# Kernel tuning notes

Measured on AMD Instinct MI355X. Metric: run time of the kernel, lower is better.

The kernel has to match this reference:

```python
import jax, jax.numpy as jnp
import numpy as np

N = 50000
E = 800000
NEG_SLOPE = 0.2


def setup_inputs() -> dict:
    key = jax.random.key(0)
    ks = jax.random.split(key, 12)
    feat = jax.random.normal(ks[0], (N, 256), dtype=jnp.float32)
    src = jax.random.randint(ks[1], (E,), 0, N, dtype=jnp.int32)
    dst = jax.random.randint(ks[2], (E,), 0, N, dtype=jnp.int32)
    # layer 1: in=256 -> H=4, D=64 (concat 256)
    W1 = jax.random.normal(ks[3], (256, 256), dtype=jnp.float32) * (1.0 / np.sqrt(256))
    attn_l1 = jax.random.normal(ks[4], (4, 64), dtype=jnp.float32) * 0.1
    attn_r1 = jax.random.normal(ks[5], (4, 64), dtype=jnp.float32) * 0.1
    bias1 = jnp.zeros((256,), dtype=jnp.float32)
    # layer 2: in=256 -> H=1, D=128
    W2 = jax.random.normal(ks[6], (256, 128), dtype=jnp.float32) * (1.0 / np.sqrt(256))
    attn_l2 = jax.random.normal(ks[7], (1, 128), dtype=jnp.float32) * 0.1
    attn_r2 = jax.random.normal(ks[8], (1, 128), dtype=jnp.float32) * 0.1
    bias2 = jnp.zeros((128,), dtype=jnp.float32)
    return {"feat": feat, "src": src, "dst": dst,
            "W1": W1, "attn_l1": attn_l1, "attn_r1": attn_r1, "bias1": bias1,
            "W2": W2, "attn_l2": attn_l2, "attn_r2": attn_r2, "bias2": bias2}


def gat_conv(feat, src, dst, W, attn_l, attn_r, bias, apply_relu):
    H, D = attn_l.shape
    n = feat.shape[0]
    ft = (feat @ W).reshape(n, H, D)                      # [N,H,D]
    el = jnp.einsum('nhd,hd->nh', ft, attn_l)             # [N,H]
    er = jnp.einsum('nhd,hd->nh', ft, attn_r)             # [N,H]
    e = el[src] + er[dst]                                 # [E,H]  u_add_v
    e = jnp.where(e > 0, e, NEG_SLOPE * e)                # leaky_relu
    # edge softmax grouped by dst
    m = jax.ops.segment_max(e, dst, num_segments=n)       # [N,H]
    ex = jnp.exp(e - m[dst])
    denom = jax.ops.segment_sum(ex, dst, num_segments=n)  # [N,H]
    a = ex / denom[dst]                                   # [E,H]
    msg = ft[src] * a[:, :, None]                         # [E,H,D]
    out = jax.ops.segment_sum(msg, dst, num_segments=n)   # [N,H,D]
    out = out + bias.reshape(1, H, D)
    out = out.reshape(n, H * D)                           # concat_out
    if apply_relu:
        out = jax.nn.relu(out)
    return out


def reference(feat, src, dst, W1, attn_l1, attn_r1, bias1, W2, attn_l2, attn_r2, bias2):
    h = gat_conv(feat, src, dst, W1, attn_l1, attn_r1, bias1, apply_relu=True)
    h = gat_conv(h, src, dst, W2, attn_l2, attn_r2, bias2, apply_relu=False)
    return h
```

## Files before the change

kernel.cpp:

```cpp
#include <hip/hip_runtime.h>
#include <hip/hip_bf16.h>

#define NEG_SLOPE 0.2f

typedef short s16x8 __attribute__((ext_vector_type(8)));
typedef float f32x4 __attribute__((ext_vector_type(4)));

__device__ __forceinline__ unsigned short f2bf(float f) {
    unsigned int u = __float_as_uint(f);
    unsigned int r = (u + 0x7fffu + ((u >> 16) & 1u)) >> 16;
    return (unsigned short)r;
}
__device__ __forceinline__ float bf2f(unsigned int us) {
    return __uint_as_float(us << 16);
}


__global__ void count_k(const int* __restrict__ dst, int* __restrict__ counts, int E) {
    int e = blockIdx.x * blockDim.x + threadIdx.x;
    if (e < E) atomicAdd(&counts[dst[e]], 1);
}

__global__ __launch_bounds__(1024) void partial_k(const int* __restrict__ counts,
                                                  int* __restrict__ part, int n) {
    __shared__ int s[16];
    int tid = threadIdx.x, lane = tid & 63, wid = tid >> 6;
    int i = blockIdx.x * 1024 + tid;
    int v = (i < n) ? counts[i] : 0;
    #pragma unroll
    for (int o = 32; o > 0; o >>= 1) v += __shfl_xor(v, o);
    if (lane == 0) s[wid] = v;
    __syncthreads();
    if (tid == 0) {
        int r = 0;
        #pragma unroll
        for (int w = 0; w < 16; w++) r += s[w];
        part[blockIdx.x] = r;
    }
}

__global__ void scanpart_k(int* __restrict__ part, int nb) {
    int tid = threadIdx.x;
    int orig = (tid < nb) ? part[tid] : 0;
    int v = orig;
    #pragma unroll
    for (int o = 1; o < 64; o <<= 1) {
        int t = __shfl_up(v, o);
        if (tid >= o) v += t;
    }
    if (tid < nb) part[tid] = v - orig;
}

__global__ __launch_bounds__(1024) void scanwrite_k(const int* __restrict__ counts,
                                                    const int* __restrict__ part,
                                                    int* __restrict__ offsets,
                                                    int* __restrict__ cursor, int n) {
    __shared__ int s_wt[16];
    int tid = threadIdx.x, lane = tid & 63, wid = tid >> 6;
    int i = blockIdx.x * 1024 + tid;
    int v = (i < n) ? counts[i] : 0;
    int incl = v;
    #pragma unroll
    for (int o = 1; o < 64; o <<= 1) {
        int t = __shfl_up(incl, o);
        if (lane >= o) incl += t;
    }
    if (lane == 63) s_wt[wid] = incl;
    __syncthreads();
    if (tid == 0) {
        int r = 0;
        #pragma unroll
        for (int w = 0; w < 16; w++) { int t = s_wt[w]; s_wt[w] = r; r += t; }
    }
    __syncthreads();
    if (i < n) {
        int excl = part[blockIdx.x] + s_wt[wid] + incl - v;
        offsets[i + 1] = excl + v;
        cursor[i] = excl;
    }
    if (blockIdx.x == 0 && tid == 0) offsets[0] = 0;
}

__global__ void fill_csr_k(const int* __restrict__ src, const int* __restrict__ dst,
                           int* __restrict__ cursor, int* __restrict__ csr_src, int E) {
    int e = blockIdx.x * blockDim.x + threadIdx.x;
    if (e < E) {
        int pos = atomicAdd(&cursor[dst[e]], 1);
        csr_src[pos] = src[e];
    }
}


__global__ __launch_bounds__(256) void gemm_k(const float* __restrict__ A,
                                              const float* __restrict__ B,
                                              unsigned short* __restrict__ Cb,
                                              int M, int K, int Nc) {
    __shared__ __align__(16) unsigned short As_hi[128][40], As_lo[128][40];
    __shared__ __align__(16) unsigned short Bs_hi[64][40],  Bs_lo[64][40];

    const int tid = threadIdx.x;
    const int lane = tid & 63, wid = tid >> 6;
    const int row0 = blockIdx.x * 128;
    const int col0 = blockIdx.y * 64;
    const int wm = (wid & 1) * 64;
    const int wn = (wid >> 1) * 32;
    const int quad = lane >> 4, mrow = lane & 15;

    const int a_r = tid >> 1;
    const int a_k = (tid & 1) * 16;
    const int b_k = tid >> 3;
    const int b_n = (tid & 7) * 8;
    const bool a_valid = (row0 + a_r) < M;

    f32x4 acc[4][2];
    #pragma unroll
    for (int i = 0; i < 4; i++)
        #pragma unroll
        for (int j = 0; j < 2; j++) acc[i][j] = f32x4{0.f, 0.f, 0.f, 0.f};

    for (int k0 = 0; k0 < K; k0 += 32) {
        float af[16];
        if (a_valid) {
            const float* ap = &A[(size_t)(row0 + a_r) * K + k0 + a_k];
            #pragma unroll
            for (int q = 0; q < 4; q++) {
                float4 t = *(const float4*)(ap + q * 4);
                af[q * 4 + 0] = t.x; af[q * 4 + 1] = t.y;
                af[q * 4 + 2] = t.z; af[q * 4 + 3] = t.w;
            }
        } else {
            #pragma unroll
            for (int q = 0; q < 16; q++) af[q] = 0.f;
        }
        unsigned int* dh = (unsigned int*)&As_hi[a_r][a_k];
        unsigned int* dl = (unsigned int*)&As_lo[a_r][a_k];
        #pragma unroll
        for (int p = 0; p < 8; p++) {
            unsigned short h0 = f2bf(af[2 * p]), h1 = f2bf(af[2 * p + 1]);
            unsigned short l0 = f2bf(af[2 * p] - bf2f(h0));
            unsigned short l1 = f2bf(af[2 * p + 1] - bf2f(h1));
            dh[p] = (unsigned int)h0 | ((unsigned int)h1 << 16);
            dl[p] = (unsigned int)l0 | ((unsigned int)l1 << 16);
        }
        {
            const float* bp = &B[(size_t)(k0 + b_k) * Nc + col0 + b_n];
            float4 t0 = *(const float4*)(bp);
            float4 t1 = *(const float4*)(bp + 4);
            float bf[8] = {t0.x, t0.y, t0.z, t0.w, t1.x, t1.y, t1.z, t1.w};
            #pragma unroll
            for (int x = 0; x < 8; x++) {
                unsigned short h = f2bf(bf[x]);
                unsigned short l = f2bf(bf[x] - bf2f(h));
                Bs_hi[b_n + x][b_k] = h;
                Bs_lo[b_n + x][b_k] = l;
            }
        }
        __syncthreads();

        s16x8 ah[4], al[4], bh[2], bl[2];
        #pragma unroll
        for (int i = 0; i < 4; i++) {
            ah[i] = *(const s16x8*)&As_hi[wm + 16 * i + mrow][quad * 8];
            al[i] = *(const s16x8*)&As_lo[wm + 16 * i + mrow][quad * 8];
        }
        #pragma unroll
        for (int j = 0; j < 2; j++) {
            bh[j] = *(const s16x8*)&Bs_hi[wn + 16 * j + mrow][quad * 8];
            bl[j] = *(const s16x8*)&Bs_lo[wn + 16 * j + mrow][quad * 8];
        }
        #pragma unroll
        for (int i = 0; i < 4; i++)
            #pragma unroll
            for (int j = 0; j < 2; j++) {
                acc[i][j] = __builtin_amdgcn_mfma_f32_16x16x32_bf16(ah[i], bh[j], acc[i][j], 0, 0, 0);
                acc[i][j] = __builtin_amdgcn_mfma_f32_16x16x32_bf16(ah[i], bl[j], acc[i][j], 0, 0, 0);
                acc[i][j] = __builtin_amdgcn_mfma_f32_16x16x32_bf16(al[i], bh[j], acc[i][j], 0, 0, 0);
            }
        __syncthreads();
    }

    #pragma unroll
    for (int i = 0; i < 4; i++) {
        #pragma unroll
        for (int j = 0; j < 2; j++) {
            int col = col0 + wn + 16 * j + mrow;
            int rbase = row0 + wm + 16 * i + quad * 4;
            #pragma unroll
            for (int r = 0; r < 4; r++) {
                int row = rbase + r;
                if (row < M) Cb[(size_t)row * Nc + col] = f2bf(acc[i][j][r]);
            }
        }
    }
}


template <int H, int D>
__global__ __launch_bounds__(256) void eler_k(const unsigned short* __restrict__ ft,
                                              const float* __restrict__ attn_l,
                                              const float* __restrict__ attn_r,
                                              float* __restrict__ el,
                                              float* __restrict__ er, int n_nodes) {
    constexpr int HD = H * D;
    constexpr int CPL = HD / 64;
    constexpr int G = 64 / H;
    __shared__ float s_al[HD], s_ar[HD];
    const int tid = threadIdx.x;
    for (int i = tid; i < HD; i += 256) { s_al[i] = attn_l[i]; s_ar[i] = attn_r[i]; }
    __syncthreads();
    const int lane = tid & 63, wid = tid >> 6;
    const int n = blockIdx.x * 4 + wid;
    if (n >= n_nodes) return;
    const int c0 = lane * CPL;
    const int head = c0 / D;
    float f[CPL];
    if constexpr (CPL == 4) {
        uint2 u = ((const uint2*)ft)[(size_t)n * (HD / 4) + lane];
        f[0] = bf2f(u.x & 0xffff); f[1] = bf2f(u.x >> 16);
        f[2] = bf2f(u.y & 0xffff); f[3] = bf2f(u.y >> 16);
    } else {
        unsigned int u = ((const unsigned int*)ft)[(size_t)n * (HD / 2) + lane];
        f[0] = bf2f(u & 0xffff); f[1] = bf2f(u >> 16);
    }
    float vl = 0.f, vr = 0.f;
    #pragma unroll
    for (int t = 0; t < CPL; t++) {
        vl = fmaf(f[t], s_al[c0 + t], vl);
        vr = fmaf(f[t], s_ar[c0 + t], vr);
    }
    #pragma unroll
    for (int o = G / 2; o > 0; o >>= 1) {
        vl += __shfl_xor(vl, o);
        vr += __shfl_xor(vr, o);
    }
    if ((lane & (G - 1)) == 0) {
        el[n * H + head] = vl;
        er[n * H + head] = vr;
    }
}


template <int H>
__device__ __forceinline__ void edge_e(const float* __restrict__ el, int sv,
                                       const float* ern, float* e) {
    if constexpr (H == 4) {
        float4 e4 = ((const float4*)el)[sv];
        float tmp[4] = {e4.x, e4.y, e4.z, e4.w};
        #pragma unroll
        for (int h = 0; h < 4; h++) {
            float t = tmp[h] + ern[h];
            e[h] = t > 0.f ? t : NEG_SLOPE * t;
        }
    } else {
        float t = el[sv] + ern[0];
        e[0] = t > 0.f ? t : NEG_SLOPE * t;
    }
}

template <int H, int CPL>
__device__ __forceinline__ void gather_edges(const unsigned short* __restrict__ ft,
                                             const int* s_src_w, const float* s_a_w,
                                             int cnt, int lane, int h_of, float* acc) {
    int i = 0;
    if constexpr (CPL == 4) {
        const uint2* fp = ((const uint2*)ft) + lane;
        for (; i + 8 <= cnt; i += 8) {
            int ss[8]; float ww[8]; uint2 uu[8];
            #pragma unroll
            for (int u = 0; u < 8; u++) { ss[u] = s_src_w[i + u]; ww[u] = s_a_w[(i + u) * H + h_of]; }
            #pragma unroll
            for (int u = 0; u < 8; u++) uu[u] = fp[(size_t)ss[u] * 64];
            #pragma unroll
            for (int u = 0; u < 8; u++) {
                acc[0] = fmaf(ww[u], bf2f(uu[u].x & 0xffff), acc[0]);
                acc[1] = fmaf(ww[u], bf2f(uu[u].x >> 16), acc[1]);
                acc[2] = fmaf(ww[u], bf2f(uu[u].y & 0xffff), acc[2]);
                acc[3] = fmaf(ww[u], bf2f(uu[u].y >> 16), acc[3]);
            }
        }
        for (; i < cnt; i++) {
            float w = s_a_w[i * H + h_of];
            uint2 u = fp[(size_t)s_src_w[i] * 64];
            acc[0] = fmaf(w, bf2f(u.x & 0xffff), acc[0]);
            acc[1] = fmaf(w, bf2f(u.x >> 16), acc[1]);
            acc[2] = fmaf(w, bf2f(u.y & 0xffff), acc[2]);
            acc[3] = fmaf(w, bf2f(u.y >> 16), acc[3]);
        }
    } else {
        const unsigned int* fp = ((const unsigned int*)ft) + lane;
        for (; i + 8 <= cnt; i += 8) {
            int ss[8]; float ww[8]; unsigned int uu[8];
            #pragma unroll
            for (int u = 0; u < 8; u++) { ss[u] = s_src_w[i + u]; ww[u] = s_a_w[(i + u) * H + h_of]; }
            #pragma unroll
            for (int u = 0; u < 8; u++) uu[u] = fp[(size_t)ss[u] * 64];
            #pragma unroll
            for (int u = 0; u < 8; u++) {
                acc[0] = fmaf(ww[u], bf2f(uu[u] & 0xffff), acc[0]);
                acc[1] = fmaf(ww[u], bf2f(uu[u] >> 16), acc[1]);
            }
        }
        for (; i < cnt; i++) {
            float w = s_a_w[i * H + h_of];
            unsigned int u = fp[(size_t)s_src_w[i] * 64];
            acc[0] = fmaf(w, bf2f(u & 0xffff), acc[0]);
            acc[1] = fmaf(w, bf2f(u >> 16), acc[1]);
        }
    }
}

template <int H, int D, bool RELU>
__global__ __launch_bounds__(256) void fagg_k(const unsigned short* __restrict__ ft,
                                              const float* __restrict__ el,
                                              const float* __restrict__ er,
                                              const int* __restrict__ offsets,
                                              const int* __restrict__ csr_src,
                                              const float* __restrict__ bias,
                                              float* __restrict__ out, int n_nodes) {
    constexpr int HD = H * D;
    constexpr int CPL = HD / 64;
    const int lane = threadIdx.x & 63;
    const int w = threadIdx.x >> 6;
    const int n = blockIdx.x * 4 + w;
    __shared__ int   s_src[4][64];
    __shared__ float s_a[4][64 * H];
    if (n >= n_nodes) return;
    const int off = offsets[n];
    const int deg = offsets[n + 1] - off;
    const int c0 = lane * CPL;
    const int h_of = c0 / D;

    float ern[H];
    #pragma unroll
    for (int h = 0; h < H; h++) ern[h] = er[n * H + h];

    float acc[CPL];
    #pragma unroll
    for (int t = 0; t < CPL; t++) acc[t] = 0.f;

    const int* s_src_w = s_src[w];
    const float* s_a_w = s_a[w];

    if (deg > 0 && deg <= 64) {
        const bool act = lane < deg;
        int sv = 0;
        float ev[H];
        #pragma unroll
        for (int h = 0; h < H; h++) ev[h] = -1e30f;
        if (act) {
            sv = csr_src[off + lane];
            edge_e<H>(el, sv, ern, ev);
        }
        float m[H];
        #pragma unroll
        for (int h = 0; h < H; h++) m[h] = ev[h];
        #pragma unroll
        for (int h = 0; h < H; h++)
            for (int o = 32; o > 0; o >>= 1) m[h] = fmaxf(m[h], __shfl_xor(m[h], o));
        float ex[H], sm[H];
        #pragma unroll
        for (int h = 0; h < H; h++) { ex[h] = act ? __expf(ev[h] - m[h]) : 0.f; sm[h] = ex[h]; }
        #pragma unroll
        for (int h = 0; h < H; h++)
            for (int o = 32; o > 0; o >>= 1) sm[h] += __shfl_xor(sm[h], o);
        if (act) {
            s_src[w][lane] = sv;
            #pragma unroll
            for (int h = 0; h < H; h++)
                s_a[w][lane * H + h] = ex[h] * (sm[h] > 0.f ? 1.f / sm[h] : 0.f);
        }
        gather_edges<H, CPL>(ft, s_src_w, s_a_w, deg, lane, h_of, acc);
    } else if (deg > 64) {
        float m[H];
        #pragma unroll
        for (int h = 0; h < H; h++) m[h] = -1e30f;
        for (int i = lane; i < deg; i += 64) {
            float e[H];
            edge_e<H>(el, csr_src[off + i], ern, e);
            #pragma unroll
            for (int h = 0; h < H; h++) m[h] = fmaxf(m[h], e[h]);
        }
        #pragma unroll
        for (int h = 0; h < H; h++)
            for (int o = 32; o > 0; o >>= 1) m[h] = fmaxf(m[h], __shfl_xor(m[h], o));
        float sm[H];
        #pragma unroll
        for (int h = 0; h < H; h++) sm[h] = 0.f;
        for (int i = lane; i < deg; i += 64) {
            float e[H];
            edge_e<H>(el, csr_src[off + i], ern, e);
            #pragma unroll
            for (int h = 0; h < H; h++) sm[h] += __expf(e[h] - m[h]);
        }
        #pragma unroll
        for (int h = 0; h < H; h++)
            for (int o = 32; o > 0; o >>= 1) sm[h] += __shfl_xor(sm[h], o);
        float inv[H];
        #pragma unroll
        for (int h = 0; h < H; h++) inv[h] = (sm[h] > 0.f) ? (1.f / sm[h]) : 0.f;
        for (int base = 0; base < deg; base += 64) {
            int cnt = min(64, deg - base);
            if (lane < cnt) {
                int sv = csr_src[off + base + lane];
                float e[H];
                edge_e<H>(el, sv, ern, e);
                s_src[w][lane] = sv;
                #pragma unroll
                for (int h = 0; h < H; h++)
                    s_a[w][lane * H + h] = __expf(e[h] - m[h]) * inv[h];
            }
            gather_edges<H, CPL>(ft, s_src_w, s_a_w, cnt, lane, h_of, acc);
        }
    }

    if constexpr (CPL == 4) {
        float4 b4 = ((const float4*)bias)[lane];
        float v0 = acc[0] + b4.x, v1 = acc[1] + b4.y, v2 = acc[2] + b4.z, v3 = acc[3] + b4.w;
        if (RELU) { v0 = fmaxf(v0, 0.f); v1 = fmaxf(v1, 0.f); v2 = fmaxf(v2, 0.f); v3 = fmaxf(v3, 0.f); }
        ((float4*)out)[(size_t)n * 64 + lane] = float4{v0, v1, v2, v3};
    } else {
        float2 b2 = ((const float2*)bias)[lane];
        float v0 = acc[0] + b2.x, v1 = acc[1] + b2.y;
        if (RELU) { v0 = fmaxf(v0, 0.f); v1 = fmaxf(v1, 0.f); }
        ((float2*)out)[(size_t)n * 64 + lane] = float2{v0, v1};
    }
}


extern "C" void kernel_launch(void* const* d_in, const int* in_sizes, int n_in,
                              void* d_out, int out_size, void* d_ws, size_t ws_size,
                              hipStream_t stream) {
    const float* feat    = (const float*)d_in[0];
    const int*   src     = (const int*)d_in[1];
    const int*   dst     = (const int*)d_in[2];
    const float* W1      = (const float*)d_in[3];
    const float* attn_l1 = (const float*)d_in[4];
    const float* attn_r1 = (const float*)d_in[5];
    const float* bias1   = (const float*)d_in[6];
    const float* W2      = (const float*)d_in[7];
    const float* attn_l2 = (const float*)d_in[8];
    const float* attn_r2 = (const float*)d_in[9];
    const float* bias2   = (const float*)d_in[10];
    float* out = (float*)d_out;

    const int N = in_sizes[0] / 256;
    const int E = in_sizes[1];
    const int NB = (N + 1023) / 1024;

    char* ws = (char*)d_ws;
    size_t o = 0;
    auto alloc = [&](size_t bytes) -> void* {
        void* p = ws + o;
        o = (o + bytes + 255) & ~(size_t)255;
        return p;
    };
    int* counts  = (int*)alloc((size_t)N * 4);
    int* cursor  = (int*)alloc((size_t)N * 4);
    int* offsets = (int*)alloc((size_t)(N + 1) * 4);
    int* part    = (int*)alloc(64 * 4);
    int* csr_src = (int*)alloc((size_t)E * 4);
    float* el1 = (float*)alloc((size_t)N * 4 * 4);
    float* er1 = (float*)alloc((size_t)N * 4 * 4);
    float* el2 = (float*)alloc((size_t)N * 4);
    float* er2 = (float*)alloc((size_t)N * 4);
    unsigned short* ft1b = (unsigned short*)alloc((size_t)N * 256 * 2);
    float* h1 = (float*)alloc((size_t)N * 256 * 4);
    unsigned short* ft2b = ft1b;

    hipMemsetAsync(counts, 0, (size_t)N * 4, stream);
    count_k<<<(E + 255) / 256, 256, 0, stream>>>(dst, counts, E);
    partial_k<<<NB, 1024, 0, stream>>>(counts, part, N);
    scanpart_k<<<1, 64, 0, stream>>>(part, NB);
    scanwrite_k<<<NB, 1024, 0, stream>>>(counts, part, offsets, cursor, N);
    fill_csr_k<<<(E + 255) / 256, 256, 0, stream>>>(src, dst, cursor, csr_src, E);

    gemm_k<<<dim3((N + 127) / 128, 256 / 64), 256, 0, stream>>>(feat, W1, ft1b, N, 256, 256);
    eler_k<4, 64><<<(N + 3) / 4, 256, 0, stream>>>(ft1b, attn_l1, attn_r1, el1, er1, N);
    fagg_k<4, 64, true><<<(N + 3) / 4, 256, 0, stream>>>(ft1b, el1, er1, offsets, csr_src, bias1, h1, N);

    gemm_k<<<dim3((N + 127) / 128, 128 / 64), 256, 0, stream>>>(h1, W2, ft2b, N, 256, 128);
    eler_k<1, 128><<<(N + 3) / 4, 256, 0, stream>>>(ft2b, attn_l2, attn_r2, el2, er2, N);
    fagg_k<1, 128, false><<<(N + 3) / 4, 256, 0, stream>>>(ft2b, el2, er2, offsets, csr_src, bias2, out, N);
}
```

Measured before the change: 402.6 us.

## Fold attention projections into GEMM, single-pass scan, prefetch gathers in aggregation

Precomputes W·attn_l and W·attn_r vectors inside the counting kernel, then has each GEMM block compute el/er directly from the fp32 input rows. This removes the separate eler kernels and changes numerics slightly, since el/er now come from fp32 rather than the bf16 outputs. The three-kernel scan is replaced by a single decoupled-lookback scan that spins on per-block flags, which relies on all scan blocks being co-resident. The aggregation kernel now prefetches the first eight neighbour feature rows before the softmax reductions to hide gather latency.

After: 401.2 us. About the same (-0.4%).

```diff
diff --git a/kernel.cpp b/kernel.cpp
--- a/kernel.cpp
+++ b/kernel.cpp
@@ -16,48 +16,51 @@
 }
 
 
-__global__ void count_k(const int* __restrict__ dst, int* __restrict__ counts, int E) {
-    int e = blockIdx.x * blockDim.x + threadIdx.x;
+__global__ void count_wl_k(const int* __restrict__ dst, int* __restrict__ counts, int E,
+                           const float* __restrict__ W1, const float* __restrict__ al1,
+                           const float* __restrict__ ar1,
+                           const float* __restrict__ W2, const float* __restrict__ al2,
+                           const float* __restrict__ ar2,
+                           float* __restrict__ wl1, float* __restrict__ wl2) {
+    if (blockIdx.x == 0) {
+        int k = threadIdx.x;
+        #pragma unroll
+        for (int h = 0; h < 4; h++) {
+            float sl = 0.f, sr = 0.f;
+            #pragma unroll 8
+            for (int d = 0; d < 64; d++) {
+                float wv = W1[k * 256 + h * 64 + d];
+                sl = fmaf(wv, al1[h * 64 + d], sl);
+                sr = fmaf(wv, ar1[h * 64 + d], sr);
+            }
+            wl1[k * 8 + h] = sl;
+            wl1[k * 8 + 4 + h] = sr;
+        }
+        float sl = 0.f, sr = 0.f;
+        #pragma unroll 8
+        for (int d = 0; d < 128; d++) {
+            float wv = W2[k * 128 + d];
+            sl = fmaf(wv, al2[d], sl);
+            sr = fmaf(wv, ar2[d], sr);
+        }
+        wl2[k * 2 + 0] = sl;
+        wl2[k * 2 + 1] = sr;
+        return;
+    }
+    int e = (blockIdx.x - 1) * 256 + threadIdx.x;
     if (e < E) atomicAdd(&counts[dst[e]], 1);
 }
 
-__global__ __launch_bounds__(1024) void partial_k(const int* __restrict__ counts,
-                                                  int* __restrict__ part, int n) {
-    __shared__ int s[16];
-    int tid = threadIdx.x, lane = tid & 63, wid = tid >> 6;
-    int i = blockIdx.x * 1024 + tid;
-    int v = (i < n) ? counts[i] : 0;
-    #pragma unroll
-    for (int o = 32; o > 0; o >>= 1) v += __shfl_xor(v, o);
-    if (lane == 0) s[wid] = v;
-    __syncthreads();
-    if (tid == 0) {
-        int r = 0;
-        #pragma unroll
-        for (int w = 0; w < 16; w++) r += s[w];
-        part[blockIdx.x] = r;
-    }
-}
-
-__global__ void scanpart_k(int* __restrict__ part, int nb) {
-    int tid = threadIdx.x;
-    int orig = (tid < nb) ? part[tid] : 0;
-    int v = orig;
-    #pragma unroll
-    for (int o = 1; o < 64; o <<= 1) {
-        int t = __shfl_up(v, o);
-        if (tid >= o) v += t;
-    }
-    if (tid < nb) part[tid] = v - orig;
-}
-
-__global__ __launch_bounds__(1024) void scanwrite_k(const int* __restrict__ counts,
-                                                    const int* __restrict__ part,
-                                                    int* __restrict__ offsets,
-                                                    int* __restrict__ cursor, int n) {
+
+__global__ __launch_bounds__(1024) void scan_k(const int* __restrict__ counts,
+                                               int* __restrict__ flags,
+                                               int* __restrict__ offsets,
+                                               int* __restrict__ cursor, int n) {
     __shared__ int s_wt[16];
-    int tid = threadIdx.x, lane = tid & 63, wid = tid >> 6;
-    int i = blockIdx.x * 1024 + tid;
+    __shared__ int s_base;
+    const int tid = threadIdx.x, lane = tid & 63, wid = tid >> 6;
+    const int bid = blockIdx.x;
+    const int i = bid * 1024 + tid;
     int v = (i < n) ? counts[i] : 0;
     int incl = v;
     #pragma unroll
@@ -71,14 +74,28 @@
         int r = 0;
         #pragma unroll
         for (int w = 0; w < 16; w++) { int t = s_wt[w]; s_wt[w] = r; r += t; }
+        atomicExch(&flags[bid], r + 1);
+        s_base = 0;
+    }
+    __syncthreads();
+    if (wid == 0) {
+        int contrib = 0;
+        if (lane < bid) {
+            int f;
+            while ((f = atomicAdd(&flags[lane], 0)) == 0) {}
+            contrib = f - 1;
+        }
+        #pragma unroll
+        for (int o = 32; o > 0; o >>= 1) contrib += __shfl_xor(contrib, o);
+        if (lane == 0) s_base = contrib;
     }
     __syncthreads();
     if (i < n) {
-        int excl = part[blockIdx.x] + s_wt[wid] + incl - v;
+        int excl = s_base + s_wt[wid] + (incl - v);
         offsets[i + 1] = excl + v;
         cursor[i] = excl;
     }
-    if (blockIdx.x == 0 && tid == 0) offsets[0] = 0;
+    if (bid == 0 && tid == 0) offsets[0] = 0;
 }
 
 __global__ void fill_csr_k(const int* __restrict__ src, const int* __restrict__ dst,
@@ -91,17 +108,24 @@
 }
 
 
+template <int MODE>
 __global__ __launch_bounds__(256) void gemm_k(const float* __restrict__ A,
                                               const float* __restrict__ B,
                                               unsigned short* __restrict__ Cb,
-                                              int M, int K, int Nc) {
+                                              int M, int K, int Nc,
+                                              const float* __restrict__ wl,
+                                              float* __restrict__ el,
+                                              float* __restrict__ er) {
     __shared__ __align__(16) unsigned short As_hi[128][40], As_lo[128][40];
     __shared__ __align__(16) unsigned short Bs_hi[64][40],  Bs_lo[64][40];
+    __shared__ float s_wla[256], s_wlb[256];
+    __shared__ float s_red[128][2];
 
     const int tid = threadIdx.x;
     const int lane = tid & 63, wid = tid >> 6;
     const int row0 = blockIdx.x * 128;
-    const int col0 = blockIdx.y * 64;
+    const int by = blockIdx.y;
+    const int col0 = by * 64;
     const int wm = (wid & 1) * 64;
     const int wn = (wid >> 1) * 32;
     const int quad = lane >> 4, mrow = lane & 15;
@@ -112,11 +136,16 @@
     const int b_n = (tid & 7) * 8;
     const bool a_valid = (row0 + a_r) < M;
 
+    if (MODE == 1) { s_wla[tid] = wl[tid * 8 + by]; s_wlb[tid] = wl[tid * 8 + 4 + by]; }
+    else           { s_wla[tid] = wl[tid * 2 + by]; }
+    __syncthreads();
+
     f32x4 acc[4][2];
     #pragma unroll
     for (int i = 0; i < 4; i++)
         #pragma unroll
         for (int j = 0; j < 2; j++) acc[i][j] = f32x4{0.f, 0.f, 0.f, 0.f};
+    float pa = 0.f, pb = 0.f;
 
     for (int k0 = 0; k0 < K; k0 += 32) {
         float af[16];
@@ -131,6 +160,11 @@
         } else {
             #pragma unroll
             for (int q = 0; q < 16; q++) af[q] = 0.f;
+        }
+        #pragma unroll
+        for (int p = 0; p < 16; p++) {
+            pa = fmaf(af[p], s_wla[k0 + a_k + p], pa);
+            if (MODE == 1) pb = fmaf(af[p], s_wlb[k0 + a_k + p], pb);
         }
         unsigned int* dh = (unsigned int*)&As_hi[a_r][a_k];
         unsigned int* dl = (unsigned int*)&As_lo[a_r][a_k];
@@ -157,11 +191,11 @@
         }
         __syncthreads();
 
-        s16x8 ah[4], al[4], bh[2], bl[2];
+        s16x8 ah[4], al4[4], bh[2], bl[2];
         #pragma unroll
         for (int i = 0; i < 4; i++) {
-            ah[i] = *(const s16x8*)&As_hi[wm + 16 * i + mrow][quad * 8];
-            al[i] = *(const s16x8*)&As_lo[wm + 16 * i + mrow][quad * 8];
+            ah[i]  = *(const s16x8*)&As_hi[wm + 16 * i + mrow][quad * 8];
+            al4[i] = *(const s16x8*)&As_lo[wm + 16 * i + mrow][quad * 8];
         }
         #pragma unroll
         for (int j = 0; j < 2; j++) {
@@ -172,11 +206,24 @@
         for (int i = 0; i < 4; i++)
             #pragma unroll
             for (int j = 0; j < 2; j++) {
-                acc[i][j] = __builtin_amdgcn_mfma_f32_16x16x32_bf16(ah[i], bh[j], acc[i][j], 0, 0, 0);
-                acc[i][j] = __builtin_amdgcn_mfma_f32_16x16x32_bf16(ah[i], bl[j], acc[i][j], 0, 0, 0);
-                acc[i][j] = __builtin_amdgcn_mfma_f32_16x16x32_bf16(al[i], bh[j], acc[i][j], 0, 0, 0);
+                acc[i][j] = __builtin_amdgcn_mfma_f32_16x16x32_bf16(ah[i],  bh[j], acc[i][j], 0, 0, 0);
+                acc[i][j] = __builtin_amdgcn_mfma_f32_16x16x32_bf16(ah[i],  bl[j], acc[i][j], 0, 0, 0);
+                acc[i][j] = __builtin_amdgcn_mfma_f32_16x16x32_bf16(al4[i], bh[j], acc[i][j], 0, 0, 0);
             }
         __syncthreads();
+    }
+
+    if (a_k == 16) { s_red[a_r][0] = pa; if (MODE == 1) s_red[a_r][1] = pb; }
+    __syncthreads();
+    if (a_k == 0 && a_valid) {
+        float ra = pa + s_red[a_r][0];
+        if (MODE == 1) {
+            float rb = pb + s_red[a_r][1];
+            el[(row0 + a_r) * 4 + by] = ra;
+            er[(row0 + a_r) * 4 + by] = rb;
+        } else {
+            (by == 0 ? el : er)[row0 + a_r] = ra;
+        }
     }
 
     #pragma unroll
@@ -191,51 +238,6 @@
                 if (row < M) Cb[(size_t)row * Nc + col] = f2bf(acc[i][j][r]);
             }
         }
-    }
-}
-
-
-template <int H, int D>
-__global__ __launch_bounds__(256) void eler_k(const unsigned short* __restrict__ ft,
-                                              const float* __restrict__ attn_l,
-                                              const float* __restrict__ attn_r,
-                                              float* __restrict__ el,
-                                              float* __restrict__ er, int n_nodes) {
-    constexpr int HD = H * D;
-    constexpr int CPL = HD / 64;
-    constexpr int G = 64 / H;
-    __shared__ float s_al[HD], s_ar[HD];
-    const int tid = threadIdx.x;
-    for (int i = tid; i < HD; i += 256) { s_al[i] = attn_l[i]; s_ar[i] = attn_r[i]; }
-    __syncthreads();
-    const int lane = tid & 63, wid = tid >> 6;
-    const int n = blockIdx.x * 4 + wid;
-    if (n >= n_nodes) return;
-    const int c0 = lane * CPL;
-    const int head = c0 / D;
-    float f[CPL];
-    if constexpr (CPL == 4) {
-        uint2 u = ((const uint2*)ft)[(size_t)n * (HD / 4) + lane];
-        f[0] = bf2f(u.x & 0xffff); f[1] = bf2f(u.x >> 16);
-        f[2] = bf2f(u.y & 0xffff); f[3] = bf2f(u.y >> 16);
-    } else {
-        unsigned int u = ((const unsigned int*)ft)[(size_t)n * (HD / 2) + lane];
-        f[0] = bf2f(u & 0xffff); f[1] = bf2f(u >> 16);
-    }
-    float vl = 0.f, vr = 0.f;
-    #pragma unroll
-    for (int t = 0; t < CPL; t++) {
-        vl = fmaf(f[t], s_al[c0 + t], vl);
-        vr = fmaf(f[t], s_ar[c0 + t], vr);
-    }
-    #pragma unroll
-    for (int o = G / 2; o > 0; o >>= 1) {
-        vl += __shfl_xor(vl, o);
-        vr += __shfl_xor(vr, o);
-    }
-    if ((lane & (G - 1)) == 0) {
-        el[n * H + head] = vl;
-        er[n * H + head] = vr;
     }
 }
 
@@ -260,16 +262,19 @@
 template <int H, int CPL>
 __device__ __forceinline__ void gather_edges(const unsigned short* __restrict__ ft,
                                              const int* s_src_w, const float* s_a_w,
-                                             int cnt, int lane, int h_of, float* acc) {
-    int i = 0;
+                                             int i0, int cnt, int lane, int h_of,
+                                             float* acc) {
+    int i = i0;
     if constexpr (CPL == 4) {
         const uint2* fp = ((const uint2*)ft) + lane;
         for (; i + 8 <= cnt; i += 8) {
             int ss[8]; float ww[8]; uint2 uu[8];
             #pragma unroll
-            for (int u = 0; u < 8; u++) { ss[u] = s_src_w[i + u]; ww[u] = s_a_w[(i + u) * H + h_of]; }
+            for (int u = 0; u < 8; u++) ss[u] = s_src_w[i + u];
             #pragma unroll
             for (int u = 0; u < 8; u++) uu[u] = fp[(size_t)ss[u] * 64];
+            #pragma unroll
+            for (int u = 0; u < 8; u++) ww[u] = s_a_w[(i + u) * H + h_of];
             #pragma unroll
             for (int u = 0; u < 8; u++) {
                 acc[0] = fmaf(ww[u], bf2f(uu[u].x & 0xffff), acc[0]);
@@ -291,9 +296,11 @@
         for (; i + 8 <= cnt; i += 8) {
             int ss[8]; float ww[8]; unsigned int uu[8];
             #pragma unroll
-            for (int u = 0; u < 8; u++) { ss[u] = s_src_w[i + u]; ww[u] = s_a_w[(i + u) * H + h_of]; }
+            for (int u = 0; u < 8; u++) ss[u] = s_src_w[i + u];
             #pragma unroll
             for (int u = 0; u < 8; u++) uu[u] = fp[(size_t)ss[u] * 64];
+            #pragma unroll
+            for (int u = 0; u < 8; u++) ww[u] = s_a_w[(i + u) * H + h_of];
             #pragma unroll
             for (int u = 0; u < 8; u++) {
                 acc[0] = fmaf(ww[u], bf2f(uu[u] & 0xffff), acc[0]);
@@ -344,12 +351,37 @@
     if (deg > 0 && deg <= 64) {
         const bool act = lane < deg;
         int sv = 0;
+        if (act) { sv = csr_src[off + lane]; s_src[w][lane] = sv; }
+        float4 elv = float4{0.f, 0.f, 0.f, 0.f};
+        float el1v = 0.f;
+        if constexpr (H == 4) { if (act) elv = ((const float4*)el)[sv]; }
+        else                  { if (act) el1v = el[sv]; }
+        const int P = deg < 8 ? deg : 8;
+        uint2 pre4[8]; unsigned int pre2[8];
+        if constexpr (CPL == 4) {
+            const uint2* fp = ((const uint2*)ft) + lane;
+            #pragma unroll
+            for (int u = 0; u < 8; u++)
+                if (u < P) { int su = __shfl(sv, u); pre4[u] = fp[(size_t)su * 64]; }
+        } else {
+            const unsigned int* fp = ((const unsigned int*)ft) + lane;
+            #pragma unroll
+            for (int u = 0; u < 8; u++)
+                if (u < P) { int su = __shfl(sv, u); pre2[u] = fp[(size_t)su * 64]; }
+        }
         float ev[H];
-        #pragma unroll
-        for (int h = 0; h < H; h++) ev[h] = -1e30f;
-        if (act) {
-            sv = csr_src[off + lane];
-            edge_e<H>(el, sv, ern, ev);
+        if constexpr (H == 4) {
+            float tmp[4] = {elv.x, elv.y, elv.z, elv.w};
+            #pragma unroll
+            for (int h = 0; h < 4; h++) {
+                float t = tmp[h] + ern[h];
+                t = t > 0.f ? t : NEG_SLOPE * t;
+                ev[h] = act ? t : -1e30f;
+            }
+        } else {
+            float t = el1v + ern[0];
+            t = t > 0.f ? t : NEG_SLOPE * t;
+            ev[0] = act ? t : -1e30f;
         }
         float m[H];
         #pragma unroll
@@ -364,12 +396,30 @@
         for (int h = 0; h < H; h++)
             for (int o = 32; o > 0; o >>= 1) sm[h] += __shfl_xor(sm[h], o);
         if (act) {
-            s_src[w][lane] = sv;
             #pragma unroll
             for (int h = 0; h < H; h++)
                 s_a[w][lane * H + h] = ex[h] * (sm[h] > 0.f ? 1.f / sm[h] : 0.f);
         }
-        gather_edges<H, CPL>(ft, s_src_w, s_a_w, deg, lane, h_of, acc);
+        if constexpr (CPL == 4) {
+            #pragma unroll
+            for (int u = 0; u < 8; u++)
+                if (u < P) {
+                    float wgt = s_a_w[u * H + h_of];
+                    acc[0] = fmaf(wgt, bf2f(pre4[u].x & 0xffff), acc[0]);
+                    acc[1] = fmaf(wgt, bf2f(pre4[u].x >> 16), acc[1]);
+                    acc[2] = fmaf(wgt, bf2f(pre4[u].y & 0xffff), acc[2]);
+                    acc[3] = fmaf(wgt, bf2f(pre4[u].y >> 16), acc[3]);
+                }
+        } else {
+            #pragma unroll
+            for (int u = 0; u < 8; u++)
+                if (u < P) {
+                    float wgt = s_a_w[u * H + h_of];
+                    acc[0] = fmaf(wgt, bf2f(pre2[u] & 0xffff), acc[0]);
+                    acc[1] = fmaf(wgt, bf2f(pre2[u] >> 16), acc[1]);
+                }
+        }
+        gather_edges<H, CPL>(ft, s_src_w, s_a_w, P, deg, lane, h_of, acc);
     } else if (deg > 64) {
         float m[H];
         #pragma unroll
@@ -409,7 +459,7 @@
                 for (int h = 0; h < H; h++)
                     s_a[w][lane * H + h] = __expf(e[h] - m[h]) * inv[h];
             }
-            gather_edges<H, CPL>(ft, s_src_w, s_a_w, cnt, lane, h_of, acc);
+            gather_edges<H, CPL>(ft, s_src_w, s_a_w, 0, cnt, lane, h_of, acc);
         }
     }
 
@@ -454,11 +504,13 @@
         o = (o + bytes + 255) & ~(size_t)255;
         return p;
     };
-    int* counts  = (int*)alloc((size_t)N * 4);
+    int* counts  = (int*)alloc((size_t)(N + 64) * 4);
+    int* flags   = counts + N;
     int* cursor  = (int*)alloc((size_t)N * 4);
     int* offsets = (int*)alloc((size_t)(N + 1) * 4);
-    int* part    = (int*)alloc(64 * 4);
     int* csr_src = (int*)alloc((size_t)E * 4);
+    float* wl1 = (float*)alloc(256 * 8 * 4);
+    float* wl2 = (float*)alloc(256 * 2 * 4);
     float* el1 = (float*)alloc((size_t)N * 4 * 4);
     float* er1 = (float*)alloc((size_t)N * 4 * 4);
     float* el2 = (float*)alloc((size_t)N * 4);
@@ -467,18 +519,19 @@
     float* h1 = (float*)alloc((size_t)N * 256 * 4);
     unsigned short* ft2b = ft1b;
 
-    hipMemsetAsync(counts, 0, (size_t)N * 4, stream);
-    count_k<<<(E + 255) / 256, 256, 0, stream>>>(dst, counts, E);
-    partial_k<<<NB, 1024, 0, stream>>>(counts, part, N);
-    scanpart_k<<<1, 64, 0, stream>>>(part, NB);
-    scanwrite_k<<<NB, 1024, 0, stream>>>(counts, part, offsets, cursor, N);
+    hipMemsetAsync(counts, 0, (size_t)(N + 64) * 4, stream);
+    count_wl_k<<<1 + (E + 255) / 256, 256, 0, stream>>>(dst, counts, E,
+        W1, attn_l1, attn_r1, W2, attn_l2, attn_r2, wl1, wl2);
+    scan_k<<<NB, 1024, 0, stream>>>(counts, flags, offsets, cursor, N);
     fill_csr_k<<<(E + 255) / 256, 256, 0, stream>>>(src, dst, cursor, csr_src, E);
 
-    gemm_k<<<dim3((N + 127) / 128, 256 / 64), 256, 0, stream>>>(feat, W1, ft1b, N, 256, 256);
-    eler_k<4, 64><<<(N + 3) / 4, 256, 0, stream>>>(ft1b, attn_l1, attn_r1, el1, er1, N);
-    fagg_k<4, 64, true><<<(N + 3) / 4, 256, 0, stream>>>(ft1b, el1, er1, offsets, csr_src, bias1, h1, N);
-
-    gemm_k<<<dim3((N + 127) / 128, 128 / 64), 256, 0, stream>>>(h1, W2, ft2b, N, 256, 128);
-    eler_k<1, 128><<<(N + 3) / 4, 256, 0, stream>>>(ft2b, attn_l2, attn_r2, el2, er2, N);
-    fagg_k<1, 128, false><<<(N + 3) / 4, 256, 0, stream>>>(ft2b, el2, er2, offsets, csr_src, bias2, out, N);
-}
+    gemm_k<1><<<dim3((N + 127) / 128, 4), 256, 0, stream>>>(feat, W1, ft1b, N, 256, 256,
+                                                            wl1, el1, er1);
+    fagg_k<4, 64, true><<<(N + 3) / 4, 256, 0, stream>>>(ft1b, el1, er1, offsets, csr_src,
+                                                         bias1, h1, N);
+
+    gemm_k<2><<<dim3((N + 127) / 128, 2), 256, 0, stream>>>(h1, W2, ft2b, N, 256, 128,
+                                                            wl2, el2, er2);
+    fagg_k<1, 128, false><<<(N + 3) / 4, 256, 0, stream>>>(ft2b, el2, er2, offsets, csr_src,
+                                                           bias2, out, N);
+}
```
